# Kernel optimization log

Hardware: AMD Instinct MI355X
Metric: run time of the kernel (lower is better)

Reference implementation:

```python
import jax, jax.numpy as jnp
import numpy as np

B, T, C, H = 2, 1024, 768, 12
D = C // H
HID = 4 * C
EPS_YAT = 1e-6
EPS_LN = 1e-6


def yat_dense(x, kernel, bias, alpha):
    # scale = (sqrt(n_out)/log(1+n_out))**alpha
    y = x @ kernel
    dist = (jnp.sum(x * x, axis=-1, keepdims=True)
            + jnp.sum(kernel * kernel, axis=0) - 2.0 * y)
    y = (y * y) / (dist + EPS_YAT)
    if bias is not None:
        y = y + bias
    n = kernel.shape[1]
    scale = (jnp.sqrt(jnp.float32(n)) / jnp.log1p(jnp.float32(n))) ** alpha
    return y * scale


def layernorm(x, scale):
    mu = jnp.mean(x, axis=-1, keepdims=True)
    var = jnp.mean((x - mu) ** 2, axis=-1, keepdims=True)
    return (x - mu) * jax.lax.rsqrt(var + EPS_LN) * scale


def rope_table(seq_len, dim):
    freqs = jnp.exp(jnp.arange(0, dim, 2, dtype=jnp.float32)
                    * (-jnp.log(10000.0) / dim))
    angles = jnp.arange(seq_len, dtype=jnp.float32)[:, None] * freqs[None, :]
    return jnp.concatenate([jnp.cos(angles), jnp.sin(angles)], axis=-1)  # [T, D]


def block_forward(x, mask, p):
    Bc, Tc, Cc = x.shape
    h = layernorm(x, p['ln1_scale'])
    qkv = yat_dense(h, p['w_qkv'], p['b_qkv'], p['a_qkv'])  # [B,T,3C]
    qkv = qkv.reshape(Bc, Tc, 3, H, D)
    q, k, v = qkv[:, :, 0], qkv[:, :, 1], qkv[:, :, 2]      # [B,T,H,D]
    rope = rope_table(Tc, D)[:, None, :]                     # [T,1,D]
    q = q * rope
    k = k * rope
    scale = 1.0 / jnp.sqrt(jnp.float32(D))
    attn = jnp.einsum('bihd,bjhd->bhij', q, k) * scale       # [B,H,T,T]
    attn = jnp.where(mask, attn, jnp.finfo(attn.dtype).min)
    attn = jax.nn.softmax(attn, axis=-1)
    o = jnp.einsum('bhij,bjhd->bihd', attn, v).reshape(Bc, Tc, Cc)
    o = yat_dense(o, p['w_ao'], p['b_ao'], p['a_ao'])
    x = x + o
    h = layernorm(x, p['ln2_scale'])
    gate = yat_dense(h, p['w_fc'], p['b_fc'], p['a_fc'])
    u = yat_dense(h, p['w_gate'], p['b_gate'], p['a_gate'])
    u = jax.nn.gelu(u) * gate
    u = yat_dense(u, p['w_proj'], p['b_proj'], p['a_proj'])
    return x + u


def setup_inputs() -> dict:
    key = jax.random.key(0)
    ks = jax.random.split(key, 8)
    x = jax.random.normal(ks[0], (B, T, C), dtype=jnp.float32)
    mask = jnp.tril(jnp.ones((T, T), dtype=bool))[None, None]  # causal [1,1,T,T]
    w = lambda k, shp: 0.02 * jax.random.normal(k, shp, dtype=jnp.float32)
    return {
        'x': x, 'mask': mask,
        'ln1_scale': jnp.ones((C,), jnp.float32),
        'w_qkv': w(ks[1], (C, 3 * C)), 'b_qkv': jnp.zeros((3 * C,), jnp.float32),
        'a_qkv': jnp.ones((1,), jnp.float32),
        'w_ao': w(ks[2], (C, C)), 'b_ao': jnp.zeros((C,), jnp.float32),
        'a_ao': jnp.ones((1,), jnp.float32),
        'ln2_scale': jnp.ones((C,), jnp.float32),
        'w_fc': w(ks[3], (C, HID)), 'b_fc': jnp.zeros((HID,), jnp.float32),
        'a_fc': jnp.ones((1,), jnp.float32),
        'w_gate': w(ks[4], (C, HID)), 'b_gate': jnp.zeros((HID,), jnp.float32),
        'a_gate': jnp.ones((1,), jnp.float32),
        'w_proj': w(ks[5], (HID, C)), 'b_proj': jnp.zeros((C,), jnp.float32),
        'a_proj': jnp.ones((1,), jnp.float32),
    }


def reference(x, mask, ln1_scale, w_qkv, b_qkv, a_qkv, w_ao, b_ao, a_ao,
              ln2_scale, w_fc, b_fc, a_fc, w_gate, b_gate, a_gate,
              w_proj, b_proj, a_proj):
    p = dict(ln1_scale=ln1_scale, w_qkv=w_qkv, b_qkv=b_qkv, a_qkv=a_qkv,
             w_ao=w_ao, b_ao=b_ao, a_ao=a_ao, ln2_scale=ln2_scale,
             w_fc=w_fc, b_fc=b_fc, a_fc=a_fc, w_gate=w_gate, b_gate=b_gate,
             a_gate=a_gate, w_proj=w_proj, b_proj=b_proj, a_proj=a_proj)
    return block_forward(x, mask, p)
```

## Files before the change

kernel.cpp:

```cpp
#include <hip/hip_runtime.h>
#include <cstdint>

#define DEVFN static __device__ __forceinline__

typedef __bf16 bf16x8 __attribute__((ext_vector_type(8)));
typedef float f32x4 __attribute__((ext_vector_type(4)));
typedef unsigned short us4 __attribute__((ext_vector_type(4)));

DEVFN unsigned short f2bf(float f) {
  unsigned u = __float_as_uint(f);
  u += 0x7fffu + ((u >> 16) & 1u);
  return (unsigned short)(u >> 16);
}
DEVFN float bf2f(unsigned short h) { return __uint_as_float(((unsigned)h) << 16); }
DEVFN void async16(const void* g, void* l) {
  __builtin_amdgcn_global_load_lds((__attribute__((address_space(1))) const void*)g,
                                   (__attribute__((address_space(3))) void*)l, 16, 0, 0);
}
DEVFN float gelu_t(float u) {
  return 0.5f * u * (1.f + tanhf(0.7978845608028654f * (u + 0.044715f * u * u * u)));
}
DEVFN int xcd_swizzle(int lin, int total) {
  return (lin & 7) * (total >> 3) + (lin >> 3);
}

__global__ __launch_bounds__(256) void k_rope(float* __restrict__ rope) {
  int g = blockIdx.x * 256 + threadIdx.x;
  int t = g >> 6, dd = g & 63, i = dd & 31;
  float fr = __expf(-0.2878231366242558f * (float)i);
  float ang = (float)t * fr;
  rope[g] = (dd < 32) ? cosf(ang) : sinf(ang);
}

struct TrArgs {
  const float* W[5]; unsigned short* Wt[5]; float* cn[5];
  int N[5]; int off[6];
};
__global__ __launch_bounds__(256) void k_transpose(TrArgs a) {
  __shared__ float tile[32][33];
  __shared__ float part[8][32];
  int lin = blockIdx.x;
  int e = 0;
  while (lin >= a.off[e + 1]) ++e;
  int local = lin - a.off[e];
  const int N = a.N[e];
  int nbx = N >> 5;
  int tn = local % nbx, tk = local / nbx;
  const float* W = a.W[e];
  unsigned short* Wt = a.Wt[e];
  float* cn = a.cn[e];
  const int K = (e == 4) ? 3072 : 768;
  int tx = threadIdx.x & 31, ty = threadIdx.x >> 5;
  float acc = 0.f;
  #pragma unroll
  for (int j = 0; j < 4; ++j) {
    int r = ty + j * 8;
    float v = W[(long)(tk * 32 + r) * N + tn * 32 + tx];
    tile[r][tx] = v;
    acc += v * v;
  }
  part[ty][tx] = acc;
  __syncthreads();
  #pragma unroll
  for (int j = 0; j < 4; ++j) {
    int rr = ty + j * 8;
    Wt[(long)(tn * 32 + rr) * K + tk * 32 + tx] = f2bf(tile[tx][rr]);
  }
  if (ty == 0) {
    float s = part[0][tx];
    #pragma unroll
    for (int jj = 1; jj < 8; ++jj) s += part[jj][tx];
    atomicAdd(&cn[tn * 32 + tx], s);
  }
}

__global__ __launch_bounds__(256) void k_ln(const float* __restrict__ x,
    const float* __restrict__ g, unsigned short* __restrict__ h, float* __restrict__ row2) {
  int row = blockIdx.x, tid = threadIdx.x;
  const float* xr = x + (long)row * 768;
  float v0 = xr[tid], v1 = xr[tid + 256], v2 = xr[tid + 512];
  float s = v0 + v1 + v2;
  float ss = v0 * v0 + v1 * v1 + v2 * v2;
  #pragma unroll
  for (int o = 32; o; o >>= 1) { s += __shfl_xor(s, o); ss += __shfl_xor(ss, o); }
  __shared__ float red[12];
  int wv = tid >> 6;
  if ((tid & 63) == 0) { red[wv] = s; red[wv + 4] = ss; }
  __syncthreads();
  s = red[0] + red[1] + red[2] + red[3];
  ss = red[4] + red[5] + red[6] + red[7];
  float mu = s * (1.f / 768.f);
  float var = ss * (1.f / 768.f) - mu * mu;
  float rs = rsqrtf(var + 1e-6f);
  float h0 = (v0 - mu) * rs * g[tid];
  float h1 = (v1 - mu) * rs * g[tid + 256];
  float h2 = (v2 - mu) * rs * g[tid + 512];
  unsigned short* hr = h + (long)row * 768;
  hr[tid] = f2bf(h0); hr[tid + 256] = f2bf(h1); hr[tid + 512] = f2bf(h2);
  float p = h0 * h0 + h1 * h1 + h2 * h2;
  #pragma unroll
  for (int o = 32; o; o >>= 1) p += __shfl_xor(p, o);
  if ((tid & 63) == 0) red[8 + wv] = p;
  __syncthreads();
  if (tid == 0) row2[row] = red[8] + red[9] + red[10] + red[11];
}

constexpr int M_QKV = 0, M_AO = 1, M_PART = 2;

struct GemmArgs {
  const unsigned short* A; const unsigned short* Bt;
  const float* arow2; const float* wcol2; const float* bias; const float* alpha;
  int N; int ks;
  const float* rope;
  unsigned short* qo; unsigned short* ko; unsigned short* vo;
  const float* xf; float* xo;
  float* part;
};

template <int MODE, int NI, int NBM, int NBN, int NZ>
__global__ __launch_bounds__(256, 4) void k_gemm(GemmArgs p) {
  __shared__ __align__(16) unsigned short As[3][2048];
  __shared__ __align__(16) unsigned short Bs[3][4096];
  const int tid = threadIdx.x, wave = tid >> 6, lane = tid & 63;
  const int quad = lane >> 4, l = lane & 15;
  constexpr int TOTAL = NBM * NBN * NZ;
  const int g = xcd_swizzle(blockIdx.x, TOTAL);
  const int bm = (g % NBM) * 64;
  const int rest = g / NBM;
  const int bn = (rest % NBN) * 128;
  const int z = rest / NBN;
  const int kb = z * (NI * 32);
  const int ks = p.ks;
  const int wm = (wave & 1) * 32, wn = (wave >> 1) * 64;
  const f32x4 fzero = {0.f, 0.f, 0.f, 0.f};
  f32x4 acc[2][4];
  #pragma unroll
  for (int i = 0; i < 2; ++i)
    #pragma unroll
    for (int j = 0; j < 4; ++j) acc[i][j] = fzero;
  const int sw = (l >> 1) & 3;

  auto stage = [&](int s, int k0) {
    {
      int ci = tid;
      int r = ci >> 2;
      int c = (ci & 3) ^ ((r >> 1) & 3);
      async16(p.A + (long)(bm + r) * ks + kb + k0 + c * 8, &As[s][ci * 8]);
    }
    #pragma unroll
    for (int it = 0; it < 2; ++it) {
      int ci = tid + it * 256;
      int r = ci >> 2;
      int c = (ci & 3) ^ ((r >> 1) & 3);
      async16(p.Bt + (long)(bn + r) * ks + kb + k0 + c * 8, &Bs[s][ci * 8]);
    }
  };
  auto compute = [&](int s) {
    bf16x8 af[2], bfv[4];
    #pragma unroll
    for (int mi = 0; mi < 2; ++mi)
      af[mi] = *(const bf16x8*)&As[s][(wm + mi * 16 + l) * 32 + ((quad ^ sw) * 8)];
    #pragma unroll
    for (int ni = 0; ni < 4; ++ni)
      bfv[ni] = *(const bf16x8*)&Bs[s][(wn + ni * 16 + l) * 32 + ((quad ^ sw) * 8)];
    #pragma unroll
    for (int mi = 0; mi < 2; ++mi)
      #pragma unroll
      for (int ni = 0; ni < 4; ++ni)
        acc[mi][ni] = __builtin_amdgcn_mfma_f32_16x16x32_bf16(af[mi], bfv[ni], acc[mi][ni], 0, 0, 0);
  };
  auto iter = [&](int s, int i) {
    if (i + 1 >= NI) { asm volatile("s_waitcnt vmcnt(0)" ::: "memory"); }
    else             { asm volatile("s_waitcnt vmcnt(3)" ::: "memory"); }
    __builtin_amdgcn_s_barrier();
    asm volatile("" ::: "memory");
    if (i + 2 < NI) stage(s == 0 ? 2 : s - 1, (i + 2) * 32);
    compute(s);
  };

  stage(0, 0);
  stage(1, 32);
  int i = 0;
  while (i < NI) {
    iter(0, i); ++i;
    iter(1, i); ++i;
    iter(2, i); ++i;
  }

  if constexpr (MODE == M_PART) {
    float* slab = p.part + (long)z * (2048 * 768);
    #pragma unroll
    for (int ni = 0; ni < 4; ++ni) {
      const int j = bn + wn + ni * 16 + l;
      #pragma unroll
      for (int mi = 0; mi < 2; ++mi) {
        const int i0 = bm + wm + mi * 16 + quad * 4;
        #pragma unroll
        for (int rg = 0; rg < 4; ++rg)
          slab[(long)(i0 + rg) * 768 + j] = acc[mi][ni][rg];
      }
    }
  } else {
    const float al = p.alpha[0];
    const float nn = (float)p.N;
    const float ys = powf(sqrtf(nn) / log1pf(nn), al);
    #pragma unroll
    for (int ni = 0; ni < 4; ++ni) {
      const int j = bn + wn + ni * 16 + l;
      const float w2 = p.wcol2[j];
      const float bj = p.bias[j];
      int s3 = 0, hh = 0, dd = 0;
      if constexpr (MODE == M_QKV) { s3 = j / 768; int rem = j - s3 * 768; hh = rem >> 6; dd = rem & 63; }
      #pragma unroll
      for (int mi = 0; mi < 2; ++mi) {
        const int i0 = bm + wm + mi * 16 + quad * 4;
        float vv[4];
        #pragma unroll
        for (int rg = 0; rg < 4; ++rg) {
          const float y = acc[mi][ni][rg];
          const float dist = p.arow2[i0 + rg] + w2 - 2.f * y + 1e-6f;
          vv[rg] = (y * y / dist + bj) * ys;
        }
        if constexpr (MODE == M_QKV) {
          int b = i0 >> 10, t0 = i0 & 1023;
          if (s3 == 2) {
            us4 pk = {f2bf(vv[0]), f2bf(vv[1]), f2bf(vv[2]), f2bf(vv[3])};
            *(us4*)&p.vo[((long)(b * 12 + hh) * 64 + dd) * 1024 + t0] = pk;
          } else {
            unsigned short* dst = (s3 == 0) ? p.qo : p.ko;
            #pragma unroll
            for (int rg = 0; rg < 4; ++rg) {
              float ro = p.rope[(t0 + rg) * 64 + dd];
              dst[((long)(b * 12 + hh) * 1024 + t0 + rg) * 64 + dd] = f2bf(vv[rg] * ro);
            }
          }
        } else {
          #pragma unroll
          for (int rg = 0; rg < 4; ++rg) {
            long idx = (long)(i0 + rg) * 768 + j;
            p.xo[idx] = p.xf[idx] + vv[rg];
          }
        }
      }
    }
  }
}

struct EpiArgs {
  const float* slab; const float* arow2; const float* wcol2;
  const float* bias; const float* alpha; const float* xo; float* outf;
};
__global__ __launch_bounds__(256) void k_proj_epi(EpiArgs p) {
  int g = blockIdx.x * 256 + threadIdx.x;
  int i = g / 192, jv = (g - i * 192) * 4;
  long base = (long)i * 768 + jv;
  f32x4 y = *(const f32x4*)(p.slab + base);
  y += *(const f32x4*)(p.slab + 1572864 + base);
  const float a2 = p.arow2[i];
  const float ys = powf(sqrtf(768.f) / log1pf(768.f), p.alpha[0]);
  f32x4 xo4 = *(const f32x4*)(p.xo + base);
  f32x4 out;
  #pragma unroll
  for (int c = 0; c < 4; ++c) {
    float yy = y[c];
    float dist = a2 + p.wcol2[jv + c] - 2.f * yy + 1e-6f;
    out[c] = xo4[c] + (yy * yy / dist + p.bias[jv + c]) * ys;
  }
  *(f32x4*)(p.outf + base) = out;
}

struct MlpArgs {
  const unsigned short* A; const unsigned short* Bf; const unsigned short* Bg;
  const float* arow2; const float* w2f; const float* w2g;
  const float* bf; const float* bg; const float* af_; const float* ag_;
  unsigned short* mlp; float* mrow2;
};

__global__ __launch_bounds__(256, 2) void k_mlp(MlpArgs p) {
  constexpr int NI = 24, K = 768;
  __shared__ __align__(16) unsigned short As[2][4096];
  __shared__ __align__(16) unsigned short Bfs[2][4096];
  __shared__ __align__(16) unsigned short Bgs[2][4096];
  const int tid = threadIdx.x, wave = tid >> 6, lane = tid & 63;
  const int quad = lane >> 4, l = lane & 15;
  const int g = xcd_swizzle(blockIdx.x, 16 * 24);
  const int bm = (g % 16) * 128, bn = (g / 16) * 128;
  const int wm = (wave & 1) * 64, wn = (wave >> 1) * 64;
  const f32x4 fzero = {0.f, 0.f, 0.f, 0.f};
  f32x4 accf[4][4], accg[4][4];
  #pragma unroll
  for (int i = 0; i < 4; ++i)
    #pragma unroll
    for (int j = 0; j < 4; ++j) { accf[i][j] = fzero; accg[i][j] = fzero; }
  const int sw = (l >> 1) & 3;

  auto stage = [&](int s, int k0) {
    #pragma unroll
    for (int it = 0; it < 2; ++it) {
      int ci = tid + it * 256;
      int r = ci >> 2;
      int c = (ci & 3) ^ ((r >> 1) & 3);
      async16(p.A  + (long)(bm + r) * K + k0 + c * 8, &As[s][ci * 8]);
      async16(p.Bf + (long)(bn + r) * K + k0 + c * 8, &Bfs[s][ci * 8]);
      async16(p.Bg + (long)(bn + r) * K + k0 + c * 8, &Bgs[s][ci * 8]);
    }
  };

  stage(0, 0);
  for (int i = 0; i < NI; ++i) {
    int s = i & 1;
    asm volatile("s_waitcnt vmcnt(0)" ::: "memory");
    __builtin_amdgcn_s_barrier();
    asm volatile("" ::: "memory");
    if (i + 1 < NI) stage(s ^ 1, (i + 1) * 32);
    bf16x8 af[4], bff[4], bfg[4];
    #pragma unroll
    for (int mi = 0; mi < 4; ++mi)
      af[mi] = *(const bf16x8*)&As[s][(wm + mi * 16 + l) * 32 + ((quad ^ sw) * 8)];
    #pragma unroll
    for (int ni = 0; ni < 4; ++ni) {
      bff[ni] = *(const bf16x8*)&Bfs[s][(wn + ni * 16 + l) * 32 + ((quad ^ sw) * 8)];
      bfg[ni] = *(const bf16x8*)&Bgs[s][(wn + ni * 16 + l) * 32 + ((quad ^ sw) * 8)];
    }
    #pragma unroll
    for (int mi = 0; mi < 4; ++mi)
      #pragma unroll
      for (int ni = 0; ni < 4; ++ni) {
        accf[mi][ni] = __builtin_amdgcn_mfma_f32_16x16x32_bf16(af[mi], bff[ni], accf[mi][ni], 0, 0, 0);
        accg[mi][ni] = __builtin_amdgcn_mfma_f32_16x16x32_bf16(af[mi], bfg[ni], accg[mi][ni], 0, 0, 0);
      }
  }

  const float ysf = powf(sqrtf(3072.f) / log1pf(3072.f), p.af_[0]);
  const float ysg = powf(sqrtf(3072.f) / log1pf(3072.f), p.ag_[0]);
  float w2f[4], w2g[4], bjf[4], bjg[4]; int js[4];
  #pragma unroll
  for (int ni = 0; ni < 4; ++ni) {
    int j = bn + wn + ni * 16 + l;
    js[ni] = j; w2f[ni] = p.w2f[j]; w2g[ni] = p.w2g[j]; bjf[ni] = p.bf[j]; bjg[ni] = p.bg[j];
  }
  #pragma unroll
  for (int mi = 0; mi < 4; ++mi) {
    #pragma unroll
    for (int rg = 0; rg < 4; ++rg) {
      const int ii = bm + wm + mi * 16 + quad * 4 + rg;
      const float a2 = p.arow2[ii];
      float rsum = 0.f;
      #pragma unroll
      for (int ni = 0; ni < 4; ++ni) {
        float yf = accf[mi][ni][rg];
        float gate = (yf * yf / (a2 + w2f[ni] - 2.f * yf + 1e-6f) + bjf[ni]) * ysf;
        float yg = accg[mi][ni][rg];
        float u  = (yg * yg / (a2 + w2g[ni] - 2.f * yg + 1e-6f) + bjg[ni]) * ysg;
        float out = gelu_t(u) * gate;
        p.mlp[(long)ii * 3072 + js[ni]] = f2bf(out);
        rsum += out * out;
      }
      #pragma unroll
      for (int o = 8; o; o >>= 1) rsum += __shfl_xor(rsum, o);
      if (l == 0) atomicAdd(&p.mrow2[ii], rsum);
    }
  }
}

__global__ __launch_bounds__(256) void k_attn(const unsigned short* __restrict__ qb,
    const unsigned short* __restrict__ kb, const unsigned short* __restrict__ vb,
    unsigned short* __restrict__ ob, float* __restrict__ orow2) {
  __shared__ __align__(16) unsigned short Qs[64 * 64];
  __shared__ __align__(16) unsigned short Ks[64 * 64];
  __shared__ __align__(16) unsigned short Vs[64 * 64];
  __shared__ __align__(16) unsigned short Ps[4 * 16 * 64];
  const int tid = threadIdx.x, wave = tid >> 6, lane = tid & 63;
  const int quad = lane >> 4, l = lane & 15;
  const int g = xcd_swizzle(blockIdx.x, 16 * 24);
  const int qt = g % 16, bh = g / 16;
  const int b = bh / 12, hh = bh % 12;
  const int q0 = qt * 64;
  const f32x4 fzero = {0.f, 0.f, 0.f, 0.f};

  const unsigned short* qg = qb + ((long)bh * 1024 + q0) * 64;
  #pragma unroll
  for (int it = 0; it < 2; ++it) {
    int ci = tid + it * 256;
    int r = ci >> 3;
    int c = (ci & 7) ^ (r & 7);
    async16(qg + (long)r * 64 + c * 8, &Qs[ci * 8]);
  }
  __builtin_amdgcn_s_waitcnt(0);
  __syncthreads();
  bf16x8 aq[2];
  #pragma unroll
  for (int ks = 0; ks < 2; ++ks)
    aq[ks] = *(const bf16x8*)&Qs[(wave * 16 + l) * 64 + (((ks * 4 + quad) ^ (l & 7)) * 8)];

  f32x4 O[4];
  float mi_[4], li[4];
  #pragma unroll
  for (int f = 0; f < 4; ++f) O[f] = fzero;
  #pragma unroll
  for (int r = 0; r < 4; ++r) { mi_[r] = -1e30f; li[r] = 0.f; }

  for (int jt = 0; jt <= qt; ++jt) {
    __syncthreads();
    const unsigned short* kg = kb + ((long)bh * 1024 + jt * 64) * 64;
    const unsigned short* vg = vb + (long)bh * 64 * 1024 + jt * 64;
    #pragma unroll
    for (int it = 0; it < 2; ++it) {
      int ci = tid + it * 256;
      int r = ci >> 3;
      int c = (ci & 7) ^ (r & 7);
      async16(kg + (long)r * 64 + c * 8, &Ks[ci * 8]);
      async16(vg + (long)r * 1024 + c * 8, &Vs[ci * 8]);
    }
    __builtin_amdgcn_s_waitcnt(0);
    __syncthreads();

    f32x4 S[4];
    #pragma unroll
    for (int f = 0; f < 4; ++f) S[f] = fzero;
    #pragma unroll
    for (int ks = 0; ks < 2; ++ks) {
      #pragma unroll
      for (int f = 0; f < 4; ++f) {
        bf16x8 bk = *(const bf16x8*)&Ks[(f * 16 + l) * 64 + (((ks * 4 + quad) ^ (l & 7)) * 8)];
        S[f] = __builtin_amdgcn_mfma_f32_16x16x32_bf16(aq[ks], bk, S[f], 0, 0, 0);
      }
    }
    const bool diag = (jt == qt);
    #pragma unroll
    for (int f = 0; f < 4; ++f)
      #pragma unroll
      for (int r = 0; r < 4; ++r) {
        float v = S[f][r] * 0.125f;
        if (diag && (f * 16 + l > wave * 16 + quad * 4 + r)) v = -1e30f;
        S[f][r] = v;
      }
    #pragma unroll
    for (int r = 0; r < 4; ++r) {
      float mx = fmaxf(fmaxf(S[0][r], S[1][r]), fmaxf(S[2][r], S[3][r]));
      #pragma unroll
      for (int o = 8; o; o >>= 1) mx = fmaxf(mx, __shfl_xor(mx, o));
      float mnew = fmaxf(mi_[r], mx);
      float alr = __expf(mi_[r] - mnew);
      float sum = 0.f;
      #pragma unroll
      for (int f = 0; f < 4; ++f) {
        float e = __expf(S[f][r] - mnew);
        S[f][r] = e;
        sum += e;
      }
      #pragma unroll
      for (int o = 8; o; o >>= 1) sum += __shfl_xor(sum, o);
      li[r] = li[r] * alr + sum;
      #pragma unroll
      for (int f = 0; f < 4; ++f) O[f][r] *= alr;
      mi_[r] = mnew;
    }
    #pragma unroll
    for (int f = 0; f < 4; ++f)
      #pragma unroll
      for (int r = 0; r < 4; ++r) {
        int i = quad * 4 + r;
        int j = f * 16 + l;
        int pch = (j >> 3) ^ (i & 7);
        Ps[wave * 1024 + i * 64 + pch * 8 + (j & 7)] = f2bf(S[f][r]);
      }
    #pragma unroll
    for (int ks = 0; ks < 2; ++ks) {
      bf16x8 ap = *(const bf16x8*)&Ps[wave * 1024 + l * 64 + (((ks * 4 + quad) ^ (l & 7)) * 8)];
      #pragma unroll
      for (int f = 0; f < 4; ++f) {
        bf16x8 bv = *(const bf16x8*)&Vs[(f * 16 + l) * 64 + (((ks * 4 + quad) ^ (l & 7)) * 8)];
        O[f] = __builtin_amdgcn_mfma_f32_16x16x32_bf16(ap, bv, O[f], 0, 0, 0);
      }
    }
  }
  #pragma unroll
  for (int f = 0; f < 4; ++f)
    #pragma unroll
    for (int r = 0; r < 4; ++r) {
      int t = q0 + wave * 16 + quad * 4 + r;
      int dd = f * 16 + l;
      float v = O[f][r] / li[r];
      ob[((long)(b * 1024 + t) * 12 + hh) * 64 + dd] = f2bf(v);
    }
  #pragma unroll
  for (int r = 0; r < 4; ++r) {
    float rsum = 0.f;
    #pragma unroll
    for (int f = 0; f < 4; ++f) { float v = O[f][r] / li[r]; rsum += v * v; }
    #pragma unroll
    for (int o = 8; o; o >>= 1) rsum += __shfl_xor(rsum, o);
    if (l == 0) {
      int t = q0 + wave * 16 + quad * 4 + r;
      atomicAdd(&orow2[b * 1024 + t], rsum);
    }
  }
}

extern "C" void kernel_launch(void* const* d_in, const int* in_sizes, int n_in,
                              void* d_out, int out_size, void* d_ws, size_t ws_size,
                              hipStream_t stream) {
  (void)in_sizes; (void)n_in; (void)out_size;
  char* w = (char*)d_ws;
  size_t off = 0;
  auto alloc = [&](size_t bytes) -> void* {
    void* p = w + off;
    off = (off + bytes + 255) & ~(size_t)255;
    return p;
  };
  float* rope            = (float*)alloc(65536 * 4);
  unsigned short* wtqkv  = (unsigned short*)alloc((size_t)2304 * 768 * 2);
  unsigned short* wtao   = (unsigned short*)alloc((size_t)768 * 768 * 2);
  unsigned short* wtfc   = (unsigned short*)alloc((size_t)3072 * 768 * 2);
  unsigned short* wtgate = (unsigned short*)alloc((size_t)3072 * 768 * 2);
  unsigned short* wtproj = (unsigned short*)alloc((size_t)768 * 3072 * 2);
  float* zeroed          = (float*)alloc(14080 * 4);
  unsigned short* h1     = (unsigned short*)alloc((size_t)2048 * 768 * 2);
  float* hrow1           = (float*)alloc(2048 * 4);
  unsigned short* qbuf   = (unsigned short*)alloc((size_t)2048 * 768 * 2);
  unsigned short* kbuf   = (unsigned short*)alloc((size_t)2048 * 768 * 2);
  unsigned short* vbuf   = (unsigned short*)alloc((size_t)2048 * 768 * 2);
  unsigned short* obuf   = (unsigned short*)alloc((size_t)2048 * 768 * 2);
  float* xo              = (float*)alloc((size_t)2048 * 768 * 4);
  unsigned short* h2     = (unsigned short*)alloc((size_t)2048 * 768 * 2);
  float* hrow2           = (float*)alloc(2048 * 4);
  unsigned short* mlp    = (unsigned short*)alloc((size_t)2048 * 3072 * 2);
  float* slabs           = (float*)alloc((size_t)2 * 2048 * 768 * 4);
  if (off > ws_size) return;

  float* wcol2  = zeroed;
  float* orow2  = zeroed + 9984;
  float* mrow2  = zeroed + 9984 + 2048;
  float* c_qkv  = wcol2 + 0;
  float* c_ao   = wcol2 + 2304;
  float* c_fc   = wcol2 + 3072;
  float* c_gate = wcol2 + 6144;
  float* c_proj = wcol2 + 9216;

  const float* xin = (const float*)d_in[0];

  hipMemsetAsync(zeroed, 0, 14080 * 4, stream);
  k_rope<<<256, 256, 0, stream>>>(rope);

  TrArgs ta;
  ta.W[0] = (const float*)d_in[3];  ta.Wt[0] = wtqkv;  ta.cn[0] = c_qkv;  ta.N[0] = 2304;
  ta.W[1] = (const float*)d_in[6];  ta.Wt[1] = wtao;   ta.cn[1] = c_ao;   ta.N[1] = 768;
  ta.W[2] = (const float*)d_in[10]; ta.Wt[2] = wtfc;   ta.cn[2] = c_fc;   ta.N[2] = 3072;
  ta.W[3] = (const float*)d_in[13]; ta.Wt[3] = wtgate; ta.cn[3] = c_gate; ta.N[3] = 3072;
  ta.W[4] = (const float*)d_in[16]; ta.Wt[4] = wtproj; ta.cn[4] = c_proj; ta.N[4] = 768;
  ta.off[0] = 0; ta.off[1] = 1728; ta.off[2] = 2304; ta.off[3] = 4608;
  ta.off[4] = 6912; ta.off[5] = 9216;
  k_transpose<<<9216, 256, 0, stream>>>(ta);

  k_ln<<<2048, 256, 0, stream>>>(xin, (const float*)d_in[2], h1, hrow1);

  GemmArgs gq = {};
  gq.A = h1; gq.Bt = wtqkv; gq.arow2 = hrow1; gq.wcol2 = c_qkv;
  gq.bias = (const float*)d_in[4]; gq.alpha = (const float*)d_in[5];
  gq.N = 2304; gq.ks = 768;
  gq.rope = rope; gq.qo = qbuf; gq.ko = kbuf; gq.vo = vbuf;
  k_gemm<M_QKV, 24, 32, 18, 1><<<576, 256, 0, stream>>>(gq);

  k_attn<<<384, 256, 0, stream>>>(qbuf, kbuf, vbuf, obuf, orow2);

  GemmArgs ga = {};
  ga.A = obuf; ga.Bt = wtao; ga.arow2 = orow2; ga.wcol2 = c_ao;
  ga.bias = (const float*)d_in[7]; ga.alpha = (const float*)d_in[8];
  ga.N = 768; ga.ks = 768;
  ga.xf = xin; ga.xo = xo;
  k_gemm<M_AO, 24, 32, 6, 1><<<192, 256, 0, stream>>>(ga);

  k_ln<<<2048, 256, 0, stream>>>(xo, (const float*)d_in[9], h2, hrow2);

  MlpArgs gm = {};
  gm.A = h2; gm.Bf = wtfc; gm.Bg = wtgate; gm.arow2 = hrow2;
  gm.w2f = c_fc; gm.w2g = c_gate;
  gm.bf = (const float*)d_in[11]; gm.bg = (const float*)d_in[14];
  gm.af_ = (const float*)d_in[12]; gm.ag_ = (const float*)d_in[15];
  gm.mlp = mlp; gm.mrow2 = mrow2;
  k_mlp<<<384, 256, 0, stream>>>(gm);

  GemmArgs gp = {};
  gp.A = mlp; gp.Bt = wtproj;
  gp.N = 768; gp.ks = 3072;
  gp.part = slabs;
  k_gemm<M_PART, 48, 32, 6, 2><<<384, 256, 0, stream>>>(gp);

  EpiArgs ge = {};
  ge.slab = slabs; ge.arow2 = mrow2; ge.wcol2 = c_proj;
  ge.bias = (const float*)d_in[17]; ge.alpha = (const float*)d_in[18];
  ge.xo = xo; ge.outf = (float*)d_out;
  k_proj_epi<<<1536, 256, 0, stream>>>(ge);
}
```

Before: 290.8 us.

## Fuse prep kernels and triple-buffer MLP and attention loads

Merges the rope table, weight transpose/column-norm, and first layernorm into one k_prep launch to cut launch overhead and let independent work overlap. Converts the MLP GEMM from double to triple buffering with partial vmcnt waits, so two stages of loads are in flight. Triple-buffers K/V in attention with prefetch two tiles ahead, and reorders the block mapping so the longest causal query tiles are scheduled first. The extra LDS (MLP goes to 72KB per block with 2 blocks/CU requested) may reduce occupancy.

```diff
diff --git a/kernel.cpp b/kernel.cpp
--- a/kernel.cpp
+++ b/kernel.cpp
@@ -24,53 +24,84 @@
   return (lin & 7) * (total >> 3) + (lin >> 3);
 }
 
-__global__ __launch_bounds__(256) void k_rope(float* __restrict__ rope) {
-  int g = blockIdx.x * 256 + threadIdx.x;
-  int t = g >> 6, dd = g & 63, i = dd & 31;
-  float fr = __expf(-0.2878231366242558f * (float)i);
-  float ang = (float)t * fr;
-  rope[g] = (dd < 32) ? cosf(ang) : sinf(ang);
-}
-
-struct TrArgs {
+struct PrepArgs {
+  float* rope;
   const float* W[5]; unsigned short* Wt[5]; float* cn[5];
   int N[5]; int off[6];
+  const float* x; const float* g1s; unsigned short* h1; float* hrow1;
 };
-__global__ __launch_bounds__(256) void k_transpose(TrArgs a) {
+__global__ __launch_bounds__(256) void k_prep(PrepArgs a) {
   __shared__ float tile[32][33];
   __shared__ float part[8][32];
-  int lin = blockIdx.x;
-  int e = 0;
-  while (lin >= a.off[e + 1]) ++e;
-  int local = lin - a.off[e];
-  const int N = a.N[e];
-  int nbx = N >> 5;
-  int tn = local % nbx, tk = local / nbx;
-  const float* W = a.W[e];
-  unsigned short* Wt = a.Wt[e];
-  float* cn = a.cn[e];
-  const int K = (e == 4) ? 3072 : 768;
-  int tx = threadIdx.x & 31, ty = threadIdx.x >> 5;
-  float acc = 0.f;
-  #pragma unroll
-  for (int j = 0; j < 4; ++j) {
-    int r = ty + j * 8;
-    float v = W[(long)(tk * 32 + r) * N + tn * 32 + tx];
-    tile[r][tx] = v;
-    acc += v * v;
-  }
-  part[ty][tx] = acc;
-  __syncthreads();
-  #pragma unroll
-  for (int j = 0; j < 4; ++j) {
-    int rr = ty + j * 8;
-    Wt[(long)(tn * 32 + rr) * K + tk * 32 + tx] = f2bf(tile[tx][rr]);
-  }
-  if (ty == 0) {
-    float s = part[0][tx];
-    #pragma unroll
-    for (int jj = 1; jj < 8; ++jj) s += part[jj][tx];
-    atomicAdd(&cn[tn * 32 + tx], s);
+  __shared__ float red[12];
+  const int bid = blockIdx.x, tid = threadIdx.x;
+  if (bid < 256) {
+    int g = bid * 256 + tid;
+    int t = g >> 6, dd = g & 63, i = dd & 31;
+    float fr = __expf(-0.2878231366242558f * (float)i);
+    float ang = (float)t * fr;
+    a.rope[g] = (dd < 32) ? cosf(ang) : sinf(ang);
+  } else if (bid < 9472) {
+    int lin = bid - 256;
+    int e = 0;
+    while (lin >= a.off[e + 1]) ++e;
+    int local = lin - a.off[e];
+    const int N = a.N[e];
+    int nbx = N >> 5;
+    int tn = local % nbx, tk = local / nbx;
+    const float* W = a.W[e];
+    unsigned short* Wt = a.Wt[e];
+    float* cn = a.cn[e];
+    const int K = (e == 4) ? 3072 : 768;
+    int tx = tid & 31, ty = tid >> 5;
+    float acc = 0.f;
+    #pragma unroll
+    for (int j = 0; j < 4; ++j) {
+      int r = ty + j * 8;
+      float v = W[(long)(tk * 32 + r) * N + tn * 32 + tx];
+      tile[r][tx] = v;
+      acc += v * v;
+    }
+    part[ty][tx] = acc;
+    __syncthreads();
+    #pragma unroll
+    for (int j = 0; j < 4; ++j) {
+      int rr = ty + j * 8;
+      Wt[(long)(tn * 32 + rr) * K + tk * 32 + tx] = f2bf(tile[tx][rr]);
+    }
+    if (ty == 0) {
+      float s = part[0][tx];
+      #pragma unroll
+      for (int jj = 1; jj < 8; ++jj) s += part[jj][tx];
+      atomicAdd(&cn[tn * 32 + tx], s);
+    }
+  } else {
+    int row = bid - 9472;
+    const float* xr = a.x + (long)row * 768;
+    float v0 = xr[tid], v1 = xr[tid + 256], v2 = xr[tid + 512];
+    float s = v0 + v1 + v2;
+    float ss = v0 * v0 + v1 * v1 + v2 * v2;
+    #pragma unroll
+    for (int o = 32; o; o >>= 1) { s += __shfl_xor(s, o); ss += __shfl_xor(ss, o); }
+    int wv = tid >> 6;
+    if ((tid & 63) == 0) { red[wv] = s; red[wv + 4] = ss; }
+    __syncthreads();
+    s = red[0] + red[1] + red[2] + red[3];
+    ss = red[4] + red[5] + red[6] + red[7];
+    float mu = s * (1.f / 768.f);
+    float var = ss * (1.f / 768.f) - mu * mu;
+    float rs = rsqrtf(var + 1e-6f);
+    float h0 = (v0 - mu) * rs * a.g1s[tid];
+    float h1 = (v1 - mu) * rs * a.g1s[tid + 256];
+    float h2 = (v2 - mu) * rs * a.g1s[tid + 512];
+    unsigned short* hr = a.h1 + (long)row * 768;
+    hr[tid] = f2bf(h0); hr[tid + 256] = f2bf(h1); hr[tid + 512] = f2bf(h2);
+    float p = h0 * h0 + h1 * h1 + h2 * h2;
+    #pragma unroll
+    for (int o = 32; o; o >>= 1) p += __shfl_xor(p, o);
+    if ((tid & 63) == 0) red[8 + wv] = p;
+    __syncthreads();
+    if (tid == 0) a.hrow1[row] = red[8] + red[9] + red[10] + red[11];
   }
 }
 
@@ -278,9 +309,9 @@
 
 __global__ __launch_bounds__(256, 2) void k_mlp(MlpArgs p) {
   constexpr int NI = 24, K = 768;
-  __shared__ __align__(16) unsigned short As[2][4096];
-  __shared__ __align__(16) unsigned short Bfs[2][4096];
-  __shared__ __align__(16) unsigned short Bgs[2][4096];
+  __shared__ __align__(16) unsigned short As[3][4096];
+  __shared__ __align__(16) unsigned short Bfs[3][4096];
+  __shared__ __align__(16) unsigned short Bgs[3][4096];
   const int tid = threadIdx.x, wave = tid >> 6, lane = tid & 63;
   const int quad = lane >> 4, l = lane & 15;
   const int g = xcd_swizzle(blockIdx.x, 16 * 24);
@@ -305,14 +336,7 @@
       async16(p.Bg + (long)(bn + r) * K + k0 + c * 8, &Bgs[s][ci * 8]);
     }
   };
-
-  stage(0, 0);
-  for (int i = 0; i < NI; ++i) {
-    int s = i & 1;
-    asm volatile("s_waitcnt vmcnt(0)" ::: "memory");
-    __builtin_amdgcn_s_barrier();
-    asm volatile("" ::: "memory");
-    if (i + 1 < NI) stage(s ^ 1, (i + 1) * 32);
+  auto compute = [&](int s) {
     bf16x8 af[4], bff[4], bfg[4];
     #pragma unroll
     for (int mi = 0; mi < 4; ++mi)
@@ -329,6 +353,23 @@
         accf[mi][ni] = __builtin_amdgcn_mfma_f32_16x16x32_bf16(af[mi], bff[ni], accf[mi][ni], 0, 0, 0);
         accg[mi][ni] = __builtin_amdgcn_mfma_f32_16x16x32_bf16(af[mi], bfg[ni], accg[mi][ni], 0, 0, 0);
       }
+  };
+  auto iter = [&](int s, int i) {
+    if (i + 1 >= NI) { asm volatile("s_waitcnt vmcnt(0)" ::: "memory"); }
+    else             { asm volatile("s_waitcnt vmcnt(6)" ::: "memory"); }
+    __builtin_amdgcn_s_barrier();
+    asm volatile("" ::: "memory");
+    if (i + 2 < NI) stage(s == 0 ? 2 : s - 1, (i + 2) * 32);
+    compute(s);
+  };
+
+  stage(0, 0);
+  stage(1, 32);
+  int i = 0;
+  while (i < NI) {
+    iter(0, i); ++i;
+    iter(1, i); ++i;
+    iter(2, i); ++i;
   }
 
   const float ysf = powf(sqrtf(3072.f) / log1pf(3072.f), p.af_[0]);
@@ -366,17 +407,30 @@
 __global__ __launch_bounds__(256) void k_attn(const unsigned short* __restrict__ qb,
     const unsigned short* __restrict__ kb, const unsigned short* __restrict__ vb,
     unsigned short* __restrict__ ob, float* __restrict__ orow2) {
-  __shared__ __align__(16) unsigned short Qs[64 * 64];
-  __shared__ __align__(16) unsigned short Ks[64 * 64];
-  __shared__ __align__(16) unsigned short Vs[64 * 64];
-  __shared__ __align__(16) unsigned short Ps[4 * 16 * 64];
+  __shared__ __align__(16) unsigned short Qs[4096];
+  __shared__ __align__(16) unsigned short Ks[3][4096];
+  __shared__ __align__(16) unsigned short Vs[3][4096];
+  __shared__ __align__(16) unsigned short Ps[4096];
   const int tid = threadIdx.x, wave = tid >> 6, lane = tid & 63;
   const int quad = lane >> 4, l = lane & 15;
   const int g = xcd_swizzle(blockIdx.x, 16 * 24);
-  const int qt = g % 16, bh = g / 16;
+  const int bh = g % 24, qt = 15 - (g / 24);
   const int b = bh / 12, hh = bh % 12;
   const int q0 = qt * 64;
   const f32x4 fzero = {0.f, 0.f, 0.f, 0.f};
+
+  auto stage_kv = [&](int s, int jt) {
+    const unsigned short* kg = kb + ((long)bh * 1024 + jt * 64) * 64;
+    const unsigned short* vg = vb + (long)bh * 64 * 1024 + jt * 64;
+    #pragma unroll
+    for (int it = 0; it < 2; ++it) {
+      int ci = tid + it * 256;
+      int r = ci >> 3;
+      int c = (ci & 7) ^ (r & 7);
+      async16(kg + (long)r * 64 + c * 8, &Ks[s][ci * 8]);
+      async16(vg + (long)r * 1024 + c * 8, &Vs[s][ci * 8]);
+    }
+  };
 
   const unsigned short* qg = qb + ((long)bh * 1024 + q0) * 64;
   #pragma unroll
@@ -386,8 +440,16 @@
     int c = (ci & 7) ^ (r & 7);
     async16(qg + (long)r * 64 + c * 8, &Qs[ci * 8]);
   }
-  __builtin_amdgcn_s_waitcnt(0);
-  __syncthreads();
+  stage_kv(0, 0);
+  if (qt >= 1) {
+    stage_kv(1, 1);
+    asm volatile("s_waitcnt vmcnt(4)" ::: "memory");
+  } else {
+    asm volatile("s_waitcnt vmcnt(0)" ::: "memory");
+  }
+  __builtin_amdgcn_s_barrier();
+  asm volatile("" ::: "memory");
+
   bf16x8 aq[2];
   #pragma unroll
   for (int ks = 0; ks < 2; ++ks)
@@ -401,19 +463,14 @@
   for (int r = 0; r < 4; ++r) { mi_[r] = -1e30f; li[r] = 0.f; }
 
   for (int jt = 0; jt <= qt; ++jt) {
-    __syncthreads();
-    const unsigned short* kg = kb + ((long)bh * 1024 + jt * 64) * 64;
-    const unsigned short* vg = vb + (long)bh * 64 * 1024 + jt * 64;
-    #pragma unroll
-    for (int it = 0; it < 2; ++it) {
-      int ci = tid + it * 256;
-      int r = ci >> 3;
-      int c = (ci & 7) ^ (r & 7);
-      async16(kg + (long)r * 64 + c * 8, &Ks[ci * 8]);
-      async16(vg + (long)r * 1024 + c * 8, &Vs[ci * 8]);
-    }
-    __builtin_amdgcn_s_waitcnt(0);
-    __syncthreads();
+    const int s = jt % 3;
+    if (jt > 0) {
+      if (jt + 1 <= qt) { asm volatile("s_waitcnt vmcnt(4)" ::: "memory"); }
+      else              { asm volatile("s_waitcnt vmcnt(0)" ::: "memory"); }
+      __builtin_amdgcn_s_barrier();
+      asm volatile("" ::: "memory");
+    }
+    if (jt + 2 <= qt) stage_kv((jt + 2) % 3, jt + 2);
 
     f32x4 S[4];
     #pragma unroll
@@ -422,7 +479,7 @@
     for (int ks = 0; ks < 2; ++ks) {
       #pragma unroll
       for (int f = 0; f < 4; ++f) {
-        bf16x8 bk = *(const bf16x8*)&Ks[(f * 16 + l) * 64 + (((ks * 4 + quad) ^ (l & 7)) * 8)];
+        bf16x8 bk = *(const bf16x8*)&Ks[s][(f * 16 + l) * 64 + (((ks * 4 + quad) ^ (l & 7)) * 8)];
         S[f] = __builtin_amdgcn_mfma_f32_16x16x32_bf16(aq[ks], bk, S[f], 0, 0, 0);
       }
     }
@@ -470,7 +527,7 @@
       bf16x8 ap = *(const bf16x8*)&Ps[wave * 1024 + l * 64 + (((ks * 4 + quad) ^ (l & 7)) * 8)];
       #pragma unroll
       for (int f = 0; f < 4; ++f) {
-        bf16x8 bv = *(const bf16x8*)&Vs[(f * 16 + l) * 64 + (((ks * 4 + quad) ^ (l & 7)) * 8)];
+        bf16x8 bv = *(const bf16x8*)&Vs[s][(f * 16 + l) * 64 + (((ks * 4 + quad) ^ (l & 7)) * 8)];
         O[f] = __builtin_amdgcn_mfma_f32_16x16x32_bf16(ap, bv, O[f], 0, 0, 0);
       }
     }
@@ -541,19 +598,18 @@
   const float* xin = (const float*)d_in[0];
 
   hipMemsetAsync(zeroed, 0, 14080 * 4, stream);
-  k_rope<<<256, 256, 0, stream>>>(rope);
-
-  TrArgs ta;
-  ta.W[0] = (const float*)d_in[3];  ta.Wt[0] = wtqkv;  ta.cn[0] = c_qkv;  ta.N[0] = 2304;
-  ta.W[1] = (const float*)d_in[6];  ta.Wt[1] = wtao;   ta.cn[1] = c_ao;   ta.N[1] = 768;
-  ta.W[2] = (const float*)d_in[10]; ta.Wt[2] = wtfc;   ta.cn[2] = c_fc;   ta.N[2] = 3072;
-  ta.W[3] = (const float*)d_in[13]; ta.Wt[3] = wtgate; ta.cn[3] = c_gate; ta.N[3] = 3072;
-  ta.W[4] = (const float*)d_in[16]; ta.Wt[4] = wtproj; ta.cn[4] = c_proj; ta.N[4] = 768;
-  ta.off[0] = 0; ta.off[1] = 1728; ta.off[2] = 2304; ta.off[3] = 4608;
-  ta.off[4] = 6912; ta.off[5] = 9216;
-  k_transpose<<<9216, 256, 0, stream>>>(ta);
-
-  k_ln<<<2048, 256, 0, stream>>>(xin, (const float*)d_in[2], h1, hrow1);
+
+  PrepArgs pa;
+  pa.rope = rope;
+  pa.W[0] = (const float*)d_in[3];  pa.Wt[0] = wtqkv;  pa.cn[0] = c_qkv;  pa.N[0] = 2304;
+  pa.W[1] = (const float*)d_in[6];  pa.Wt[1] = wtao;   pa.cn[1] = c_ao;   pa.N[1] = 768;
+  pa.W[2] = (const float*)d_in[10]; pa.Wt[2] = wtfc;   pa.cn[2] = c_fc;   pa.N[2] = 3072;
+  pa.W[3] = (const float*)d_in[13]; pa.Wt[3] = wtgate; pa.cn[3] = c_gate; pa.N[3] = 3072;
+  pa.W[4] = (const float*)d_in[16]; pa.Wt[4] = wtproj; pa.cn[4] = c_proj; pa.N[4] = 768;
+  pa.off[0] = 0; pa.off[1] = 1728; pa.off[2] = 2304; pa.off[3] = 4608;
+  pa.off[4] = 6912; pa.off[5] = 9216;
+  pa.x = xin; pa.g1s = (const float*)d_in[2]; pa.h1 = h1; pa.hrow1 = hrow1;
+  k_prep<<<11520, 256, 0, stream>>>(pa);
 
   GemmArgs gq = {};
   gq.A = h1; gq.Bt = wtqkv; gq.arow2 = hrow1; gq.wcol2 = c_qkv;
```

Result: faster. 281.1 us (-3.3%).
